# Kernel tuning notes

Hardware: AMD Instinct MI355X
Metric: run time of the kernel (lower is better)

The kernel has to match this reference:

```python
import jax, jax.numpy as jnp
import numpy as np


def _positional_embedding(C, M, dtype):
    # pe[pos, 0::2] = sin(pos*div), pe[pos, 1::2] = cos(pos*div)
    pos = jnp.arange(M, dtype=jnp.float32)[:, None]                      # [M,1]
    div = jnp.exp(jnp.arange(0, C, 2, dtype=jnp.float32) * (-np.log(10000.0) / C))  # [C/2]
    ang = pos * div                                                      # [M,C/2]
    pe = jnp.stack([jnp.sin(ang), jnp.cos(ang)], axis=-1).reshape(M, C)  # interleave
    return pe.T.astype(dtype)                                            # [C,M]


def setup_inputs() -> dict:
    key = jax.random.key(0)
    k1, k2, k3 = jax.random.split(key, 3)
    B, C, M, K = 64, 512, 1024, 5
    h_in = jax.random.normal(k1, (B, C, 1, M), dtype=jnp.float32)
    conv_w = jax.random.normal(k2, (C, K), dtype=jnp.float32) * 0.1
    conv_b = jax.random.normal(k3, (C,), dtype=jnp.float32) * 0.1
    return {"h_in": h_in, "conv_w": conv_w, "conv_b": conv_b}


def reference(h_in, conv_w, conv_b):
    B, C, _, M = h_in.shape
    K = conv_w.shape[1]
    p = (K - 1) // 2
    dt = h_in.dtype

    hb = h_in                                              # pre-PE copy
    pe = _positional_embedding(C, M, dt)                   # [C,M]
    x = h_in + pe[None, :, None, :]                        # [B,C,1,M]

    # adaptive avg pool to 1 over (H,W)
    y = jnp.mean(x, axis=(2, 3))                           # [B,C]
    # unfold along channel axis with padding p, window K
    y_pad = jnp.pad(y, ((0, 0), (p, p)))                   # [B,C+2p]
    idx = jnp.arange(C)[:, None] + jnp.arange(K)[None, :]  # [C,K]
    y_unf = y_pad[:, idx]                                  # [B,C,K]
    # grouped conv1d -> per-channel dot over window, then sigmoid gate
    gate = jax.nn.sigmoid(jnp.einsum('bck,ck->bc', y_unf, conv_w) + conv_b)  # [B,C]

    h = x * gate[:, :, None, None]                         # dropout = identity (eval)

    hs = h[:, :, 0, :]                                     # [B,C,M]
    hbs = hb[:, :, 0, :]                                   # [B,C,M]
    I_hat = (jnp.eye(M, dtype=dt) / M) - (1.0 / (M * M))   # [M,M] centering matrix

    t1 = jnp.einsum('bcm,mn->bcn', hs, I_hat)
    t2 = jnp.einsum('bcm,mn->bcn', hbs, I_hat)
    cov = (jnp.einsum('bcn,bdn->bcd', t1, hs)
           + jnp.einsum('bcn,bdn->bcd', t2, hbs)
           + jnp.eye(C, dtype=dt) * 1e-8)                  # [B,C,C]
    return cov
```

## Files before the change

kernel.cpp:

```cpp
#include <hip/hip_runtime.h>
#include <math.h>

#define B_N 64
#define C_N 512
#define M_N 1024
#define K_W 2048

typedef __attribute__((ext_vector_type(8))) short bf16x8;
typedef __attribute__((ext_vector_type(4))) float f32x4;

__device__ __forceinline__ unsigned short f2b(float f) {
  unsigned int x = __builtin_bit_cast(unsigned int, f);
  unsigned int lsb = (x >> 16) & 1u;
  x += 0x7fffu + lsb;
  return (unsigned short)(x >> 16);
}

typedef __attribute__((address_space(1))) const unsigned int gas_uint;
typedef __attribute__((address_space(3))) unsigned int las_uint;
__device__ __forceinline__ void async_ld(const void* g, const void* l) {
  __builtin_amdgcn_global_load_lds((gas_uint*)(uintptr_t)g,
                                   (las_uint*)(unsigned int)(uintptr_t)l, 16, 0, 0);
}

__global__ void k_pe(float* __restrict__ pe, float* __restrict__ pesum) {
  int c = blockIdx.x, m = threadIdx.x;
  float freq = expf((float)(c & ~1) * (-9.210340371976184f / 512.0f));
  float ang = (float)m * freq;
  float v = (c & 1) ? cosf(ang) : sinf(ang);
  pe[c * M_N + m] = v;
  float s = v;
  for (int off = 32; off; off >>= 1) s += __shfl_down(s, off);
  __shared__ float ws[16];
  if ((m & 63) == 0) ws[m >> 6] = s;
  __syncthreads();
  if (m < 16) {
    float t = ws[m];
    for (int off = 8; off; off >>= 1) t += __shfl_down(t, off);
    if (m == 0) pesum[c] = t;
  }
}

__global__ void k_rs(const float* __restrict__ src, float* __restrict__ rb) {
  size_t e = ((size_t)blockIdx.x * 256 + threadIdx.x) * 8;
  const float4* s4 = (const float4*)(src + e);
  float4 v0 = s4[0], v1 = s4[1];
  float s = v0.x + v0.y + v0.z + v0.w + v1.x + v1.y + v1.z + v1.w;
  for (int off = 32; off; off >>= 1) s += __shfl_down(s, off);
  if ((threadIdx.x & 63) == 0) atomicAdd(&rb[e >> 10], s);
}

__global__ void k_gate(const float* __restrict__ wp, const float* __restrict__ bp,
                       const float* __restrict__ rb0, const float* __restrict__ pesum,
                       float* __restrict__ u, float* __restrict__ rbF,
                       float* __restrict__ gateF) {
  int idx = blockIdx.x * 256 + threadIdx.x;
  int b = idx >> 9, c = idx & (C_N - 1);
  float rbv = rb0[idx];
  float rx = rbv + pesum[c];
  float acc = 0.f;
  for (int k = 0; k < 5; ++k) {
    int cc = c + k - 2;
    if (cc < 0 || cc >= C_N) continue;
    float y = (rb0[b * C_N + cc] + pesum[cc]) * (1.0f / 1024.0f);
    acc += y * wp[c * 5 + k];
  }
  float g = 1.0f / (1.0f + expf(-(acc + bp[c])));
  gateF[idx] = g;
  u[idx] = g * rx;
  rbF[idx] = rbv;
}

__global__ void k_x(float* __restrict__ hbase, const float* __restrict__ pe,
                    const float* __restrict__ gateF) {
  int row = blockIdx.x;
  int c = row & (C_N - 1), t = threadIdx.x;
  float* rp = hbase + (size_t)row * M_N;
  float4 h4 = ((const float4*)rp)[t];
  float4 p4 = ((const float4*)(pe + (size_t)c * M_N))[t];
  float g = gateF[row];
  union { uint2 v; unsigned short us[4]; } H, X;
  H.us[0] = f2b(h4.x); H.us[1] = f2b(h4.y); H.us[2] = f2b(h4.z); H.us[3] = f2b(h4.w);
  X.us[0] = f2b(g * (h4.x + p4.x)); X.us[1] = f2b(g * (h4.y + p4.y));
  X.us[2] = f2b(g * (h4.z + p4.z)); X.us[3] = f2b(g * (h4.w + p4.w));
  __syncthreads();
  unsigned short* wr = (unsigned short*)rp;
  ((uint2*)wr)[t] = H.v;
  ((uint2*)(wr + M_N))[t] = X.v;
}

__global__ __launch_bounds__(256, 2)
void k_cov(const unsigned short* __restrict__ W, const float* __restrict__ aux,
           float* __restrict__ out, int b0) {
  __shared__ unsigned short tiles[2][2][128 * 32];
  int t = threadIdx.x, lane = t & 63, w = t >> 6;
  int bid = blockIdx.x;
  int xcd = bid & 7, i5 = bid >> 3;
  int b = b0 + xcd * 4 + (i5 >> 4);
  int s = i5 & 15;
  int cblk = (s >> 2) * 128, dblk = (s & 3) * 128;

  int rowbase = (w & 1) ? dblk : cblk;
  int half = w >> 1;
  int gcol = (lane & 3) ^ ((lane >> 3) & 3);
  const unsigned short* srcp = W + (size_t)b * (C_N * K_W)
      + (size_t)(rowbase + half * 64 + (lane >> 2)) * K_W + gcol * 8;
  int ldst = half * 2048;

  int wr = (w >> 1) * 64, wc = (w & 1) * 64;
  int fr = lane & 15, kc = lane >> 4;
  int fcol = (kc ^ ((fr >> 1) & 3)) * 8;

  f32x4 acc[4][4];
  const f32x4 z = {0.f, 0.f, 0.f, 0.f};
  for (int i = 0; i < 4; i++) for (int j = 0; j < 4; j++) acc[i][j] = z;

  for (int g = 0; g < 4; g++)
    async_ld(srcp + (size_t)g * (16 * K_W), &tiles[0][w & 1][ldst + g * 512]);
  __syncthreads();

  for (int it = 0; it < 64; ++it) {
    int cur = it & 1;
    if (it < 63) {
      const unsigned short* sp = srcp + (it + 1) * 32;
      for (int g = 0; g < 4; g++)
        async_ld(sp + (size_t)g * (16 * K_W), &tiles[cur ^ 1][w & 1][ldst + g * 512]);
    }
    bf16x8 bf[4];
    for (int j = 0; j < 4; j++)
      bf[j] = *(const bf16x8*)&tiles[cur][1][(wc + j * 16 + fr) * 32 + fcol];
    for (int i = 0; i < 4; i++) {
      bf16x8 af = *(const bf16x8*)&tiles[cur][0][(wr + i * 16 + fr) * 32 + fcol];
      for (int j = 0; j < 4; j++)
        acc[i][j] = __builtin_amdgcn_mfma_f32_16x16x32_bf16(af, bf[j], acc[i][j], 0, 0, 0);
    }
    __syncthreads();
  }

  const float invM = 1.0f / 1024.0f, invM2 = invM * invM;
  const float* ub = aux + (size_t)b * C_N;
  const float* rbb = aux + (size_t)B_N * C_N + (size_t)b * C_N;
  for (int i = 0; i < 4; i++)
    for (int r = 0; r < 4; r++) {
      int c = cblk + wr + i * 16 + kc * 4 + r;
      float uc = ub[c], rbc = rbb[c];
      for (int j = 0; j < 4; j++) {
        int d = dblk + wc + j * 16 + fr;
        float v = acc[i][j][r] * invM - (uc * ub[d] + rbc * rbb[d]) * invM2;
        if (c == d) v += 1e-8f;
        out[((size_t)b * C_N + c) * C_N + d] = v;
      }
    }
}

extern "C" void kernel_launch(void* const* d_in, const int* in_sizes, int n_in,
                              void* d_out, int out_size, void* d_ws, size_t ws_size,
                              hipStream_t stream) {
  const float* h32 = (const float*)d_in[0];
  const float* conv_w = (const float*)d_in[1];
  const float* conv_b = (const float*)d_in[2];
  char* OUT = (char*)d_out;
  char* HIN = (char*)d_in[0];

  char* AUXA = OUT + (48ull << 20);
  float* uA    = (float*)(AUXA);
  float* rbA   = (float*)(AUXA + (128 << 10));
  float* gateF = (float*)(AUXA + (256 << 10));
  float* rb0   = (float*)(AUXA + (384 << 10));
  float* pesum = (float*)(AUXA + (512 << 10));
  float* peF   = (float*)(OUT + (49ull << 20));
  char* AUXB = HIN;

  hipMemsetAsync(rb0, 0, 128 << 10, stream);
  k_pe<<<C_N, 1024, 0, stream>>>(peF, pesum);
  k_rs<<<16384, 256, 0, stream>>>(h32, rb0);
  k_gate<<<(B_N * C_N) / 256, 256, 0, stream>>>(conv_w, conv_b, rb0, pesum,
                                                uA, rbA, gateF);
  k_x<<<B_N * C_N, 256, 0, stream>>>((float*)HIN, peF, gateF);

  k_cov<<<512, 256, 0, stream>>>((const unsigned short*)HIN, uA, (float*)d_out, 0);
  hipMemcpyAsync(AUXB, AUXA, 256 << 10, hipMemcpyDeviceToDevice, stream);
  k_cov<<<512, 256, 0, stream>>>((const unsigned short*)HIN, (const float*)AUXB,
                                 (float*)d_out, 32);
}
```

Measured before the change: 327.3 us.

## Deepen k_cov LDS pipeline to four stages with explicit waitcnt scheduling

The covariance GEMM kernel moves from a double-buffered LDS ring to a four-slot ring with three tiles in flight. A single barrier per step is guarded by explicit vmcnt waits, and all fragment loads are issued before the MFMA block, which runs at raised wave priority. The aim is to hide global-to-LDS latency and cut one barrier per iteration. LDS use doubles to 64KB per block, which may reduce occupancy below the two blocks per CU that the launch bounds request.

```diff
diff --git a/kernel.cpp b/kernel.cpp
--- a/kernel.cpp
+++ b/kernel.cpp
@@ -89,10 +89,41 @@
   ((uint2*)(wr + M_N))[t] = X.v;
 }
 
+__device__ __forceinline__ void cov_stage(unsigned short (*tl)[128 * 32],
+                                          const unsigned short* srcp, int wsel,
+                                          int ldst) {
+  for (int g = 0; g < 4; g++)
+    async_ld(srcp + (size_t)g * (16 * K_W), &tl[wsel][ldst + g * 512]);
+}
+
+template <int VM, bool STG>
+__device__ __forceinline__ void cov_step(
+    unsigned short (*tiles)[2][128 * 32], int it, const unsigned short* srcp,
+    int wsel, int ldst, int wr, int wc, int fr, int fcol, f32x4 (&acc)[4][4]) {
+  asm volatile("s_waitcnt vmcnt(%0)" ::"n"(VM) : "memory");
+  __builtin_amdgcn_sched_barrier(0);
+  __builtin_amdgcn_s_barrier();
+  __builtin_amdgcn_sched_barrier(0);
+  int cur = it & 3;
+  bf16x8 bf[4], af[4];
+  for (int j = 0; j < 4; j++)
+    bf[j] = *(const bf16x8*)&tiles[cur][1][(wc + j * 16 + fr) * 32 + fcol];
+  for (int i = 0; i < 4; i++)
+    af[i] = *(const bf16x8*)&tiles[cur][0][(wr + i * 16 + fr) * 32 + fcol];
+  if (STG) cov_stage(tiles[(it + 3) & 3], srcp + (size_t)(it + 3) * 32, wsel, ldst);
+  asm volatile("s_waitcnt lgkmcnt(0)" ::: "memory");
+  __builtin_amdgcn_sched_barrier(0);
+  __builtin_amdgcn_s_setprio(1);
+  for (int i = 0; i < 4; i++)
+    for (int j = 0; j < 4; j++)
+      acc[i][j] = __builtin_amdgcn_mfma_f32_16x16x32_bf16(af[i], bf[j], acc[i][j], 0, 0, 0);
+  __builtin_amdgcn_s_setprio(0);
+}
+
 __global__ __launch_bounds__(256, 2)
 void k_cov(const unsigned short* __restrict__ W, const float* __restrict__ aux,
            float* __restrict__ out, int b0) {
-  __shared__ unsigned short tiles[2][2][128 * 32];
+  __shared__ unsigned short tiles[4][2][128 * 32];
   int t = threadIdx.x, lane = t & 63, w = t >> 6;
   int bid = blockIdx.x;
   int xcd = bid & 7, i5 = bid >> 3;
@@ -101,7 +132,7 @@
   int cblk = (s >> 2) * 128, dblk = (s & 3) * 128;
 
   int rowbase = (w & 1) ? dblk : cblk;
-  int half = w >> 1;
+  int half = w >> 1, wsel = w & 1;
   int gcol = (lane & 3) ^ ((lane >> 3) & 3);
   const unsigned short* srcp = W + (size_t)b * (C_N * K_W)
       + (size_t)(rowbase + half * 64 + (lane >> 2)) * K_W + gcol * 8;
@@ -115,27 +146,14 @@
   const f32x4 z = {0.f, 0.f, 0.f, 0.f};
   for (int i = 0; i < 4; i++) for (int j = 0; j < 4; j++) acc[i][j] = z;
 
-  for (int g = 0; g < 4; g++)
-    async_ld(srcp + (size_t)g * (16 * K_W), &tiles[0][w & 1][ldst + g * 512]);
-  __syncthreads();
-
-  for (int it = 0; it < 64; ++it) {
-    int cur = it & 1;
-    if (it < 63) {
-      const unsigned short* sp = srcp + (it + 1) * 32;
-      for (int g = 0; g < 4; g++)
-        async_ld(sp + (size_t)g * (16 * K_W), &tiles[cur ^ 1][w & 1][ldst + g * 512]);
-    }
-    bf16x8 bf[4];
-    for (int j = 0; j < 4; j++)
-      bf[j] = *(const bf16x8*)&tiles[cur][1][(wc + j * 16 + fr) * 32 + fcol];
-    for (int i = 0; i < 4; i++) {
-      bf16x8 af = *(const bf16x8*)&tiles[cur][0][(wr + i * 16 + fr) * 32 + fcol];
-      for (int j = 0; j < 4; j++)
-        acc[i][j] = __builtin_amdgcn_mfma_f32_16x16x32_bf16(af, bf[j], acc[i][j], 0, 0, 0);
-    }
-    __syncthreads();
-  }
+  for (int s0 = 0; s0 < 3; ++s0)
+    cov_stage(tiles[s0], srcp + (size_t)s0 * 32, wsel, ldst);
+
+  for (int it = 0; it < 61; ++it)
+    cov_step<8, true>(tiles, it, srcp, wsel, ldst, wr, wc, fr, fcol, acc);
+  cov_step<8, false>(tiles, 61, srcp, wsel, ldst, wr, wc, fr, fcol, acc);
+  cov_step<4, false>(tiles, 62, srcp, wsel, ldst, wr, wc, fr, fcol, acc);
+  cov_step<0, false>(tiles, 63, srcp, wsel, ldst, wr, wc, fr, fcol, acc);
 
   const float invM = 1.0f / 1024.0f, invM2 = invM * invM;
   const float* ub = aux + (size_t)b * C_N;
```

Result: no change. 329.3 us (+0.6%).
